# Kernel tuning notes

Hardware: AMD Instinct MI355X
Metric: run time of the kernel (lower is better)

The kernel has to match this reference:

```python
import jax, jax.numpy as jnp
import numpy as np
import math

B, S, HID = 2, 2048, 512
NH, NKV, HD = 8, 2, 256
ROT = 64          # partial_rotary_factor 0.25 * head_dim 256
ROPE_THETA = 10000000.0
EPS = 1e-6


def _rms_norm(x, w):
    # zero-centered RMSNorm: x / rms * (1 + w)
    rms = jnp.sqrt(jnp.mean(x * x, axis=-1, keepdims=True) + EPS)
    return x / rms * (1.0 + w)


def _partial_rope(x, cos, sin):
    # x: [B,S,H,HD]; cos/sin: [S, ROT//2]
    xr = x[..., :ROT].reshape(*x.shape[:-1], ROT // 2, 2)
    a, b = xr[..., 0], xr[..., 1]
    c = cos[None, :, None, :]
    s = sin[None, :, None, :]
    rot = jnp.stack([a * c - b * s, a * s + b * c], axis=-1).reshape(*x.shape[:-1], ROT)
    return jnp.concatenate([rot, x[..., ROT:]], axis=-1)


def setup_inputs() -> dict:
    key = jax.random.key(0)
    ks = jax.random.split(key, 6)
    x = jax.random.normal(ks[0], (B, S, HID), dtype=jnp.float32)
    # real RoPE frequencies
    inv_freq = 1.0 / (ROPE_THETA ** (np.arange(0, ROT, 2, dtype=np.float32) / ROT))
    t = np.arange(S, dtype=np.float32)
    angles = np.outer(t, inv_freq)  # [S, ROT//2]
    cos = jnp.asarray(np.cos(angles), dtype=jnp.float32)
    sin = jnp.asarray(np.sin(angles), dtype=jnp.float32)
    # additive causal mask [S,S]
    mask = jnp.where(jnp.tril(jnp.ones((S, S), dtype=bool)), 0.0, -1e9).astype(jnp.float32)
    sc = 0.02
    wq = jax.random.normal(ks[1], (HID, NH * HD), dtype=jnp.float32) * sc
    wk = jax.random.normal(ks[2], (HID, NKV * HD), dtype=jnp.float32) * sc
    wv = jax.random.normal(ks[3], (HID, NKV * HD), dtype=jnp.float32) * sc
    wo = jax.random.normal(ks[4], (NH * HD, HID), dtype=jnp.float32) * sc
    q_norm_w = jnp.zeros((HD,), dtype=jnp.float32)
    k_norm_w = jnp.zeros((HD,), dtype=jnp.float32)
    return {"x": x, "cos": cos, "sin": sin, "mask": mask,
            "wq": wq, "wk": wk, "wv": wv, "wo": wo,
            "q_norm_w": q_norm_w, "k_norm_w": k_norm_w}


def reference(x, cos, sin, mask, wq, wk, wv, wo, q_norm_w, k_norm_w):
    b, s, _ = x.shape
    groups = NH // NKV
    q = (x @ wq).reshape(b, s, NH, HD)
    k = (x @ wk).reshape(b, s, NKV, HD)
    v = (x @ wv).reshape(b, s, NKV, HD)
    q = _partial_rope(_rms_norm(q, q_norm_w), cos, sin)
    k = _partial_rope(_rms_norm(k, k_norm_w), cos, sin)
    # GQA: broadcast kv heads to NH
    k = jnp.repeat(k, groups, axis=2)  # [b,s,NH,HD]
    v = jnp.repeat(v, groups, axis=2)
    scale = math.sqrt(HD)
    scores = jnp.einsum('bqhd,bkhd->bhqk', q, k) / scale
    scores = scores + mask[None, None, :, :]
    attn = jax.nn.softmax(scores, axis=-1)
    out = jnp.einsum('bhqk,bkhd->bqhd', attn, v).reshape(b, s, NH * HD)
    return out @ wo
```

## Files before the change

### kernel.cpp

```cpp
#include <hip/hip_runtime.h>

#define S_LEN 2048
#define NHQ 8
#define NKV 2
#define HD 256
#define KVB 32

typedef __attribute__((ext_vector_type(8))) short bf16x8;
typedef __attribute__((ext_vector_type(4))) short bf16x4;
typedef __attribute__((ext_vector_type(4))) float f32x4;
typedef __attribute__((ext_vector_type(16))) float f32x16;
typedef __attribute__((ext_vector_type(4))) unsigned u32x4;

__device__ __forceinline__ short f2bf(float f) {
    unsigned u = __builtin_bit_cast(unsigned, f);
    u += 0x7FFFu + ((u >> 16) & 1u);
    return (short)(u >> 16);
}
__device__ __forceinline__ float bf2f(short s) {
    unsigned u = ((unsigned)(unsigned short)s) << 16;
    return __builtin_bit_cast(float, u);
}
__device__ __forceinline__ unsigned cvtpk(float a, float b) {
    unsigned r;
    asm("v_cvt_pk_bf16_f32 %0, %1, %2" : "=v"(r) : "v"(a), "v"(b));
    return r;
}
__device__ __forceinline__ void gload16(const short* g, short* l) {
    __builtin_amdgcn_global_load_lds((const __attribute__((address_space(1))) unsigned*)g,
                                     (__attribute__((address_space(3))) unsigned*)l, 16, 0, 0);
}
__device__ __forceinline__ float bperm(int srclane, float v) {
    return __builtin_bit_cast(float,
        __builtin_amdgcn_ds_bpermute(srclane * 4, __builtin_bit_cast(int, v)));
}

__global__ __launch_bounds__(256) void cvt_kernel(const float* __restrict__ in,
                                                  short* __restrict__ out, int n) {
    int i = (blockIdx.x * 256 + threadIdx.x) * 4;
    if (i + 3 < n) {
        float4 f = *(const float4*)(in + i);
        bf16x4 o;
        o[0] = f2bf(f.x); o[1] = f2bf(f.y); o[2] = f2bf(f.z); o[3] = f2bf(f.w);
        *(bf16x4*)(out + i) = o;
    }
}

__global__ __launch_bounds__(256) void wt_kernel(const float* __restrict__ in,
                                                 short* __restrict__ out,
                                                 int K, int N) {
    __shared__ short tile[64][72];
    int n0 = blockIdx.x * 64, k0 = blockIdx.y * 64;
    int t = threadIdx.x;
    #pragma unroll
    for (int i = 0; i < 16; i++) {
        int flat = i * 256 + t; int r = flat >> 6, c = flat & 63;
        tile[r][c] = f2bf(in[(long)(k0 + r) * N + n0 + c]);
    }
    __syncthreads();
    #pragma unroll
    for (int i = 0; i < 16; i++) {
        int flat = i * 256 + t; int r = flat >> 6, c = flat & 63;
        out[(long)(n0 + r) * K + k0 + c] = tile[c][r];
    }
}

template<int BN, int WRITE_BF16>
__global__ __launch_bounds__(256) void gemm_bt(const short* __restrict__ A,
                                               const short* __restrict__ Bt,
                                               void* __restrict__ Cv,
                                               int M, int N, int K) {
    constexpr int NI = BN / 32;
    __shared__ short As[128 * 32];
    __shared__ short Bs[BN * 32];
    const int t = threadIdx.x;
    const int lane = t & 63, w = t >> 6;
    const int lr = lane & 15, lg = lane >> 4;
    const int m0 = blockIdx.y * 128, n0 = blockIdx.x * BN;
    const int wm = (w >> 1) * 64, wn = (w & 1) * (BN / 2);

    f32x4 acc[4][NI];
    #pragma unroll
    for (int i = 0; i < 4; i++)
        #pragma unroll
        for (int j = 0; j < NI; j++) acc[i][j] = (f32x4){0.f, 0.f, 0.f, 0.f};

    for (int k0 = 0; k0 < K; k0 += 32) {
        __syncthreads();
        #pragma unroll
        for (int r = 0; r < 2; r++) {
            int sbase = r * 2048 + w * 512;
            int srow = (sbase + lane * 8) >> 5, scol = (sbase + lane * 8) & 31;
            gload16(A + (long)(m0 + srow) * K + k0 + scol, &As[sbase]);
        }
        #pragma unroll
        for (int r = 0; r < BN / 64; r++) {
            int sbase = r * 2048 + w * 512;
            int srow = (sbase + lane * 8) >> 5, scol = (sbase + lane * 8) & 31;
            gload16(Bt + (long)(n0 + srow) * K + k0 + scol, &Bs[sbase]);
        }
        __syncthreads();
        bf16x8 af[4], bfr[NI];
        #pragma unroll
        for (int mi = 0; mi < 4; mi++)
            af[mi] = *(const bf16x8*)&As[(wm + mi * 16 + lr) * 32 + lg * 8];
        #pragma unroll
        for (int ni = 0; ni < NI; ni++)
            bfr[ni] = *(const bf16x8*)&Bs[(wn + ni * 16 + lr) * 32 + lg * 8];
        #pragma unroll
        for (int mi = 0; mi < 4; mi++)
            #pragma unroll
            for (int ni = 0; ni < NI; ni++)
                acc[mi][ni] = __builtin_amdgcn_mfma_f32_16x16x32_bf16(af[mi], bfr[ni], acc[mi][ni], 0, 0, 0);
    }
    #pragma unroll
    for (int mi = 0; mi < 4; mi++)
    #pragma unroll
    for (int ni = 0; ni < NI; ni++)
    #pragma unroll
    for (int r = 0; r < 4; r++) {
        long row = m0 + wm + mi * 16 + lg * 4 + r;
        long col = n0 + wn + ni * 16 + lr;
        float v = acc[mi][ni][r];
        if (WRITE_BF16) ((short*)Cv)[row * N + col] = f2bf(v);
        else            ((float*)Cv)[row * N + col] = v;
    }
}

__global__ __launch_bounds__(256) void norm_rope_kernel(
    const short* __restrict__ in, short* __restrict__ out,
    const float* __restrict__ w, const float* __restrict__ cosb,
    const float* __restrict__ sinb, int H, long ldin, long cofs,
    long ob, long oh, long os, float scale) {
    int vec = blockIdx.x * 4 + (threadIdx.x >> 6);
    int lane = threadIdx.x & 63;
    int token = vec / H, head = vec % H;
    int b = token / S_LEN, s = token % S_LEN;

    bf16x4 xv = *(const bf16x4*)(in + (long)token * ldin + cofs + head * 256 + lane * 4);
    float x0 = bf2f(xv[0]), x1 = bf2f(xv[1]), x2 = bf2f(xv[2]), x3 = bf2f(xv[3]);
    float ss = x0 * x0 + x1 * x1 + x2 * x2 + x3 * x3;
    #pragma unroll
    for (int m = 1; m < 64; m <<= 1) ss += __shfl_xor(ss, m);
    float inv = rsqrtf(ss * (1.f / 256.f) + 1e-6f);

    float4 wv = *(const float4*)(w + lane * 4);
    float y0 = x0 * inv * (1.f + wv.x);
    float y1 = x1 * inv * (1.f + wv.y);
    float y2 = x2 * inv * (1.f + wv.z);
    float y3 = x3 * inv * (1.f + wv.w);

    if (lane < 16) {
        float2 c = *(const float2*)&cosb[s * 32 + lane * 2];
        float2 sn = *(const float2*)&sinb[s * 32 + lane * 2];
        float a0 = y0 * c.x - y1 * sn.x, b0 = y0 * sn.x + y1 * c.x;
        float a1 = y2 * c.y - y3 * sn.y, b1 = y2 * sn.y + y3 * c.y;
        y0 = a0; y1 = b0; y2 = a1; y3 = b1;
    }
    y0 *= scale; y1 *= scale; y2 *= scale; y3 *= scale;
    long oidx = (long)b * ob + (long)head * oh + (long)s * os + lane * 4;
    bf16x4 o; o[0] = f2bf(y0); o[1] = f2bf(y1); o[2] = f2bf(y2); o[3] = f2bf(y3);
    *(bf16x4*)(out + oidx) = o;
}

__global__ __launch_bounds__(256) void transpose_v_kernel(const short* __restrict__ C,
                                                          short* __restrict__ vr) {
    __shared__ short tile[64][65];
    int s0 = blockIdx.x * 64, d0 = blockIdx.y * 64;
    int bkv = blockIdx.z; int b = bkv >> 1, kv = bkv & 1;
    int t = threadIdx.x;
    #pragma unroll
    for (int i = 0; i < 16; i++) {
        int flat = i * 256 + t; int si = flat >> 6, di = flat & 63;
        tile[si][di] = C[(long)(b * S_LEN + s0 + si) * 3072 + 2560 + kv * 256 + d0 + di];
    }
    __syncthreads();
    #pragma unroll
    for (int i = 0; i < 16; i++) {
        int flat = i * 256 + t; int di = flat >> 6, si = flat & 63;
        vr[(long)(bkv * 256 + d0 + di) * S_LEN + s0 + si] = tile[si][di];
    }
}

__global__ __launch_bounds__(256, 2) void flash_kernel(const short* __restrict__ Cq,
                                                       const short* __restrict__ Kt,
                                                       const short* __restrict__ Vt,
                                                       short* __restrict__ O,
                                                       const float* __restrict__ qnw,
                                                       const float* __restrict__ cosb,
                                                       const float* __restrict__ sinb) {
    __shared__ __align__(16) char smem[66048];

    int idx = blockIdx.x;
    int half = idx >> 8, rm = idx & 255;
    int xcd = rm & 7, slot = rm >> 3;
    int bh = xcd * 2 + (slot & 1);
    int jj = slot >> 1;
    int j  = half ? jj : (31 - jj);
    int h = bh & 7, b = bh >> 3;
    int kv = h >> 2;
    int t = threadIdx.x, lane = t & 63, w = t >> 6;
    int g = w >> 1, p = w & 1;
    int ln = lane & 31, hi = lane >> 5;
    int q0 = j * 64 + g * 32;
    int qg = q0 + ln;

    const short* Kb = Kt + (long)(b * NKV + kv) * S_LEN * HD;
    const short* Vb = Vt + (long)(b * NKV + kv) * HD * S_LEN;

    auto stageK = [&](int ph2) {
        #pragma unroll
        for (int pp = 0; pp < 2; pp++) {
            int k0s = (2 * ph2 + pp) * KVB;
            short* Ktile = (short*)(smem + pp * 16384);
            #pragma unroll
            for (int c = 0; c < 4; c++) {
                int o = c * 4096 + w * 1024 + lane * 16;
                int key = o >> 9, db = o & 511;
                gload16(Kb + (long)(k0s + key) * HD + ((db ^ ((key & 7) << 4)) >> 1),
                        Ktile + (c * 4096 + w * 1024) / 2);
            }
        }
    };
    auto stageV = [&](int ph2) {
        #pragma unroll
        for (int pp = 0; pp < 2; pp++) {
            int k0s = (2 * ph2 + pp) * KVB;
            short* Vtile = (short*)(smem + 32768 + pp * 16384);
            #pragma unroll
            for (int c = 0; c < 4; c++) {
                int o = c * 4096 + w * 1024 + lane * 16;
                int d = o >> 6, kb = o & 63;
                gload16(Vb + (long)d * S_LEN + k0s + ((kb ^ ((d & 6) << 3)) >> 1),
                        Vtile + (c * 4096 + w * 1024) / 2);
            }
        }
    };

    stageK(0); stageV(0);

    bf16x8 qf[16];
    {
        const short* qrow = Cq + (long)(b * S_LEN + qg) * 3072 + h * 256 + hi * 8;
        #pragma unroll
        for (int dc = 0; dc < 16; dc++) qf[dc] = *(const bf16x8*)&qrow[dc * 16];
        float ss = 0.f;
        #pragma unroll
        for (int dc = 0; dc < 16; dc++)
            #pragma unroll
            for (int e = 0; e < 8; e++) { float v = bf2f(qf[dc][e]); ss += v * v; }
        ss += __shfl_xor(ss, 32);
        float inv = rsqrtf(ss * (1.f / 256.f) + 1e-6f);
        #pragma unroll
        for (int dc = 0; dc < 16; dc++) {
            float y[8];
            float4 w0 = *(const float4*)&qnw[dc * 16 + hi * 8];
            float4 w1 = *(const float4*)&qnw[dc * 16 + hi * 8 + 4];
            y[0] = bf2f(qf[dc][0]) * inv * (1.f + w0.x);
            y[1] = bf2f(qf[dc][1]) * inv * (1.f + w0.y);
            y[2] = bf2f(qf[dc][2]) * inv * (1.f + w0.z);
            y[3] = bf2f(qf[dc][3]) * inv * (1.f + w0.w);
            y[4] = bf2f(qf[dc][4]) * inv * (1.f + w1.x);
            y[5] = bf2f(qf[dc][5]) * inv * (1.f + w1.y);
            y[6] = bf2f(qf[dc][6]) * inv * (1.f + w1.z);
            y[7] = bf2f(qf[dc][7]) * inv * (1.f + w1.w);
            if (dc < 4) {
                float4 c4 = *(const float4*)&cosb[qg * 32 + dc * 8 + hi * 4];
                float4 s4 = *(const float4*)&sinb[qg * 32 + dc * 8 + hi * 4];
                float a, bb;
                a = y[0]; bb = y[1]; y[0] = a * c4.x - bb * s4.x; y[1] = a * s4.x + bb * c4.x;
                a = y[2]; bb = y[3]; y[2] = a * c4.y - bb * s4.y; y[3] = a * s4.y + bb * c4.y;
                a = y[4]; bb = y[5]; y[4] = a * c4.z - bb * s4.z; y[5] = a * s4.z + bb * c4.z;
                a = y[6]; bb = y[7]; y[6] = a * c4.w - bb * s4.w; y[7] = a * s4.w + bb * c4.w;
            }
            bf16x8 o;
            #pragma unroll
            for (int e = 0; e < 8; e++) o[e] = f2bf(y[e] * 0.0625f);
            qf[dc] = o;
        }
    }

    f32x16 acc[8];
    #pragma unroll
    for (int i = 0; i < 8; i++)
        #pragma unroll
        for (int r = 0; r < 16; r++) acc[i][r] = 0.f;
    float m = -1e30f, l = 0.f;

    for (int ph = 0; ph <= j; ph++) {
        const bool last = (ph == j);
        asm volatile("s_waitcnt vmcnt(8)" ::: "memory");
        __builtin_amdgcn_s_barrier();
        int k0 = (2 * ph + p) * KVB;
        bool act = (k0 <= q0 + 31);

        f32x16 s;
        if (act) {
            const char* Ks = (const char*)smem + p * 16384;
            f32x16 sA, sB;
            #pragma unroll
            for (int r = 0; r < 16; r++) { sA[r] = 0.f; sB[r] = 0.f; }
            __builtin_amdgcn_s_setprio(1);
            #pragma unroll
            for (int dc = 0; dc < 16; dc += 2) {
                int kb0 = (dc * 32 + hi * 16) ^ ((ln & 7) << 4);
                int kb1 = ((dc + 1) * 32 + hi * 16) ^ ((ln & 7) << 4);
                bf16x8 kf0 = *(const bf16x8*)(Ks + ln * 512 + kb0);
                bf16x8 kf1 = *(const bf16x8*)(Ks + ln * 512 + kb1);
                sA = __builtin_amdgcn_mfma_f32_32x32x16_bf16(kf0, qf[dc],     sA, 0, 0, 0);
                sB = __builtin_amdgcn_mfma_f32_32x32x16_bf16(kf1, qf[dc + 1], sB, 0, 0, 0);
            }
            __builtin_amdgcn_s_setprio(0);
            #pragma unroll
            for (int r = 0; r < 16; r++) s[r] = sA[r] + sB[r];
        }
        __builtin_amdgcn_s_barrier();
        if (!last) stageK(ph + 1);
        __builtin_amdgcn_sched_barrier(0);

        bf16x8 pa0, pa1;
        if (act) {
            if (k0 + KVB - 1 > q0) {
                #pragma unroll
                for (int r = 0; r < 16; r++) {
                    int key_g = k0 + (r & 3) + 8 * (r >> 2) + 4 * hi;
                    if (key_g > qg) s[r] = -1e30f;
                }
            }
            float mt = s[0];
            #pragma unroll
            for (int r = 1; r < 16; r++) mt = fmaxf(mt, s[r]);
            mt = fmaxf(mt, __shfl_xor(mt, 32));
            float mn = m;
            if (!__all(mt <= m + 8.f)) {
                mn = fmaxf(m, mt);
                float f = __expf(m - mn);
                m = mn;
                float fr[16];
                #pragma unroll
                for (int r = 0; r < 16; r++)
                    fr[r] = bperm((r & 3) + 8 * (r >> 2) + 4 * hi, f);
                #pragma unroll
                for (int i = 0; i < 8; i++)
                    #pragma unroll
                    for (int r = 0; r < 16; r++) acc[i][r] *= fr[r];
                l *= f;
            }
            float pr[16], ps = 0.f;
            #pragma unroll
            for (int r = 0; r < 16; r++) { pr[r] = __expf(s[r] - mn); ps += pr[r]; }
            ps += __shfl_xor(ps, 32);
            l += ps;

            unsigned pw[8];
            #pragma unroll
            for (int kc = 0; kc < 2; kc++) {
                unsigned X = cvtpk(pr[kc * 8 + 0], pr[kc * 8 + 1]);
                unsigned Y = cvtpk(pr[kc * 8 + 4], pr[kc * 8 + 5]);
                unsigned Z = cvtpk(pr[kc * 8 + 2], pr[kc * 8 + 3]);
                unsigned W = cvtpk(pr[kc * 8 + 6], pr[kc * 8 + 7]);
                asm volatile("v_permlane32_swap_b32 %0, %1" : "+v"(X), "+v"(Y));
                asm volatile("v_permlane32_swap_b32 %0, %1" : "+v"(Z), "+v"(W));
                pw[kc * 4 + 0] = X; pw[kc * 4 + 1] = Z;
                pw[kc * 4 + 2] = Y; pw[kc * 4 + 3] = W;
            }
            u32x4 w0v = {pw[0], pw[1], pw[2], pw[3]};
            u32x4 w1v = {pw[4], pw[5], pw[6], pw[7]};
            pa0 = __builtin_bit_cast(bf16x8, w0v);
            pa1 = __builtin_bit_cast(bf16x8, w1v);
        }

        if (last) { asm volatile("s_waitcnt vmcnt(0)" ::: "memory"); }
        else      { asm volatile("s_waitcnt vmcnt(8)" ::: "memory"); }
        __builtin_amdgcn_s_barrier();

        if (act) {
            const char* Vs = (const char*)smem + 32768 + p * 16384;
            __builtin_amdgcn_s_setprio(1);
            #pragma unroll
            for (int db = 0; db < 8; db++) {
                int drow = db * 32 + ln;
                int sw = (drow & 6) << 3;
                bf16x8 vf0 = *(const bf16x8*)(Vs + drow * 64 + ((hi * 16) ^ sw));
                bf16x8 vf1 = *(const bf16x8*)(Vs + drow * 64 + ((32 + hi * 16) ^ sw));
                acc[db] = __builtin_amdgcn_mfma_f32_32x32x16_bf16(pa0, vf0, acc[db], 0, 0, 0);
                acc[db] = __builtin_amdgcn_mfma_f32_32x32x16_bf16(pa1, vf1, acc[db], 0, 0, 0);
            }
            __builtin_amdgcn_s_setprio(0);
        }
        __builtin_amdgcn_s_barrier();
        if (!last) stageV(ph + 1);
    }

    float* accb = (float*)smem;
    float* mlb  = (float*)(smem + 65536);
    if (p == 1) {
        #pragma unroll
        for (int db = 0; db < 8; db++)
            #pragma unroll
            for (int r = 0; r < 16; r++)
                accb[g * 8192 + (db * 16 + r) * 64 + hi * 32 + ln] = acc[db][r];
        if (hi == 0) { mlb[g * 32 + ln] = m; mlb[64 + g * 32 + ln] = l; }
    }
    __syncthreads();
    if (p == 0) {
        float m1 = mlb[g * 32 + ln], l1 = mlb[64 + g * 32 + ln];
        float M  = fmaxf(m, m1);
        float f0 = __expf(m - M), f1 = __expf(m1 - M);
        float lt = l * f0 + l1 * f1;
        float w0 = f0 / lt, w1 = f1 / lt;
        float fr0[16], fr1[16];
        #pragma unroll
        for (int r = 0; r < 16; r++) {
            int crow = (r & 3) + 8 * (r >> 2) + 4 * hi;
            fr0[r] = bperm(crow, w0);
            fr1[r] = bperm(crow, w1);
        }
        #pragma unroll
        for (int db = 0; db < 8; db++)
            #pragma unroll
            for (int r = 0; r < 16; r++) {
                float a1 = accb[g * 8192 + (db * 16 + r) * 64 + hi * 32 + ln];
                int qrow = q0 + (r & 3) + 8 * (r >> 2) + 4 * hi;
                O[(long)(b * S_LEN + qrow) * 2048 + h * HD + db * 32 + ln] =
                    f2bf(acc[db][r] * fr0[r] + a1 * fr1[r]);
            }
    }
}

extern "C" void kernel_launch(void* const* d_in, const int* in_sizes, int n_in,
                              void* d_out, int out_size, void* d_ws, size_t ws_size,
                              hipStream_t stream) {
    const float* x    = (const float*)d_in[0];
    const float* cosb = (const float*)d_in[1];
    const float* sinb = (const float*)d_in[2];
    const float* wq   = (const float*)d_in[4];
    const float* wk   = (const float*)d_in[5];
    const float* wv   = (const float*)d_in[6];
    const float* wo   = (const float*)d_in[7];
    const float* qnw  = (const float*)d_in[8];
    const float* knw  = (const float*)d_in[9];
    float* out = (float*)d_out;

    char* ws = (char*)d_ws;
    short* xb   = (short*)(ws + 0);
    short* wfus = (short*)(ws + 4194304);
    short* wot  = (short*)(ws + 7340032);
    short* C    = (short*)(ws + 9437184);
    short* ao   = (short*)(ws + 34603008);
    short* kr   = (short*)(ws + 51380224);
    short* vr   = (short*)(ws + 55574528);

    cvt_kernel<<<2048, 256, 0, stream>>>(x, xb, 2097152);
    wt_kernel<<<dim3(32, 8), 256, 0, stream>>>(wq, wfus,              512, 2048);
    wt_kernel<<<dim3(8, 8),  256, 0, stream>>>(wk, wfus + 2048 * 512, 512, 512);
    wt_kernel<<<dim3(8, 8),  256, 0, stream>>>(wv, wfus + 2560 * 512, 512, 512);
    wt_kernel<<<dim3(8, 32), 256, 0, stream>>>(wo, wot, 2048, 512);

    gemm_bt<128, 1><<<dim3(24, 32), 256, 0, stream>>>(xb, wfus, C, 4096, 3072, 512);

    norm_rope_kernel<<<2048, 256, 0, stream>>>(C, kr, knw, cosb, sinb, 2,
                                               3072L, 2048L, 1048576L, 524288L, 256L, 1.0f);
    transpose_v_kernel<<<dim3(32, 4, 4), 256, 0, stream>>>(C, vr);

    flash_kernel<<<512, 256, 0, stream>>>(C, kr, vr, ao, qnw, cosb, sinb);

    gemm_bt<64, 0><<<dim3(8, 32), 256, 0, stream>>>(ao, wot, out, 4096, 512, 2048);
}
```

Baseline: 201.8 us.

## Merge K and V staging into one load phase per iteration

Replaces the split K/V staging, where K for the next step was loaded during softmax and V during the PV phase, with one combined stage issued after each step's full compute. Each iteration now waits for all loads, computes QK, softmax and PV without an intermediate barrier, then issues the next K and V loads together. This drops two barriers and a waitcnt per iteration, but removes the overlap between next-tile loads and the current compute, since the wait is vmcnt(0) right after the loads are issued.

```diff
diff --git a/kernel.cpp b/kernel.cpp
--- a/kernel.cpp
+++ b/kernel.cpp
@@ -208,28 +208,18 @@
     const short* Kb = Kt + (long)(b * NKV + kv) * S_LEN * HD;
     const short* Vb = Vt + (long)(b * NKV + kv) * HD * S_LEN;
 
-    auto stageK = [&](int ph2) {
+    auto stage = [&](int ph2) {
         #pragma unroll
         for (int pp = 0; pp < 2; pp++) {
             int k0s = (2 * ph2 + pp) * KVB;
             short* Ktile = (short*)(smem + pp * 16384);
+            short* Vtile = (short*)(smem + 32768 + pp * 16384);
             #pragma unroll
             for (int c = 0; c < 4; c++) {
                 int o = c * 4096 + w * 1024 + lane * 16;
                 int key = o >> 9, db = o & 511;
                 gload16(Kb + (long)(k0s + key) * HD + ((db ^ ((key & 7) << 4)) >> 1),
                         Ktile + (c * 4096 + w * 1024) / 2);
-            }
-        }
-    };
-    auto stageV = [&](int ph2) {
-        #pragma unroll
-        for (int pp = 0; pp < 2; pp++) {
-            int k0s = (2 * ph2 + pp) * KVB;
-            short* Vtile = (short*)(smem + 32768 + pp * 16384);
-            #pragma unroll
-            for (int c = 0; c < 4; c++) {
-                int o = c * 4096 + w * 1024 + lane * 16;
                 int d = o >> 6, kb = o & 63;
                 gload16(Vb + (long)d * S_LEN + k0s + ((kb ^ ((d & 6) << 3)) >> 1),
                         Vtile + (c * 4096 + w * 1024) / 2);
@@ -237,7 +227,7 @@
         }
     };
 
-    stageK(0); stageV(0);
+    stage(0);
 
     bf16x8 qf[16];
     {
@@ -284,112 +274,100 @@
     #pragma unroll
     for (int i = 0; i < 8; i++)
         #pragma unroll
-        for (int r = 0; r < 16; r++) acc[i][r] = 0.f;
+        for (int jj2 = 0; jj2 < 16; jj2++) acc[i][jj2] = 0.f;
     float m = -1e30f, l = 0.f;
 
+    auto compute = [&](int k0) {
+        const char* Ks = (const char*)smem + p * 16384;
+        const char* Vs = (const char*)smem + 32768 + p * 16384;
+        f32x16 sA, sB;
+        #pragma unroll
+        for (int r = 0; r < 16; r++) { sA[r] = 0.f; sB[r] = 0.f; }
+        __builtin_amdgcn_s_setprio(1);
+        #pragma unroll
+        for (int dc = 0; dc < 16; dc += 2) {
+            int kb0 = (dc * 32 + hi * 16) ^ ((ln & 7) << 4);
+            int kb1 = ((dc + 1) * 32 + hi * 16) ^ ((ln & 7) << 4);
+            bf16x8 kf0 = *(const bf16x8*)(Ks + ln * 512 + kb0);
+            bf16x8 kf1 = *(const bf16x8*)(Ks + ln * 512 + kb1);
+            sA = __builtin_amdgcn_mfma_f32_32x32x16_bf16(kf0, qf[dc],     sA, 0, 0, 0);
+            sB = __builtin_amdgcn_mfma_f32_32x32x16_bf16(kf1, qf[dc + 1], sB, 0, 0, 0);
+        }
+        __builtin_amdgcn_s_setprio(0);
+        f32x16 s;
+        #pragma unroll
+        for (int r = 0; r < 16; r++) s[r] = sA[r] + sB[r];
+
+        if (k0 + KVB - 1 > q0) {
+            #pragma unroll
+            for (int r = 0; r < 16; r++) {
+                int key_g = k0 + (r & 3) + 8 * (r >> 2) + 4 * hi;
+                if (key_g > qg) s[r] = -1e30f;
+            }
+        }
+        float mt = s[0];
+        #pragma unroll
+        for (int r = 1; r < 16; r++) mt = fmaxf(mt, s[r]);
+        mt = fmaxf(mt, __shfl_xor(mt, 32));
+        float mn = m;
+        if (!__all(mt <= m + 8.f)) {
+            mn = fmaxf(m, mt);
+            float f = __expf(m - mn);
+            m = mn;
+            float fr[16];
+            #pragma unroll
+            for (int r = 0; r < 16; r++)
+                fr[r] = bperm((r & 3) + 8 * (r >> 2) + 4 * hi, f);
+            #pragma unroll
+            for (int i = 0; i < 8; i++)
+                #pragma unroll
+                for (int r = 0; r < 16; r++) acc[i][r] *= fr[r];
+            l *= f;
+        }
+        float pr[16], ps = 0.f;
+        #pragma unroll
+        for (int r = 0; r < 16; r++) { pr[r] = __expf(s[r] - mn); ps += pr[r]; }
+        ps += __shfl_xor(ps, 32);
+        l += ps;
+
+        unsigned pw[8];
+        #pragma unroll
+        for (int kc = 0; kc < 2; kc++) {
+            unsigned X = cvtpk(pr[kc * 8 + 0], pr[kc * 8 + 1]);
+            unsigned Y = cvtpk(pr[kc * 8 + 4], pr[kc * 8 + 5]);
+            unsigned Z = cvtpk(pr[kc * 8 + 2], pr[kc * 8 + 3]);
+            unsigned W = cvtpk(pr[kc * 8 + 6], pr[kc * 8 + 7]);
+            asm volatile("v_permlane32_swap_b32 %0, %1" : "+v"(X), "+v"(Y));
+            asm volatile("v_permlane32_swap_b32 %0, %1" : "+v"(Z), "+v"(W));
+            pw[kc * 4 + 0] = X; pw[kc * 4 + 1] = Z;
+            pw[kc * 4 + 2] = Y; pw[kc * 4 + 3] = W;
+        }
+        u32x4 w0v = {pw[0], pw[1], pw[2], pw[3]};
+        u32x4 w1v = {pw[4], pw[5], pw[6], pw[7]};
+        bf16x8 pa0 = __builtin_bit_cast(bf16x8, w0v);
+        bf16x8 pa1 = __builtin_bit_cast(bf16x8, w1v);
+
+        __builtin_amdgcn_s_setprio(1);
+        #pragma unroll
+        for (int db = 0; db < 8; db++) {
+            int drow = db * 32 + ln;
+            int sw = (drow & 6) << 3;
+            bf16x8 vf0 = *(const bf16x8*)(Vs + drow * 64 + ((hi * 16) ^ sw));
+            bf16x8 vf1 = *(const bf16x8*)(Vs + drow * 64 + ((32 + hi * 16) ^ sw));
+            acc[db] = __builtin_amdgcn_mfma_f32_32x32x16_bf16(pa0, vf0, acc[db], 0, 0, 0);
+            acc[db] = __builtin_amdgcn_mfma_f32_32x32x16_bf16(pa1, vf1, acc[db], 0, 0, 0);
+        }
+        __builtin_amdgcn_s_setprio(0);
+    };
+
     for (int ph = 0; ph <= j; ph++) {
-        const bool last = (ph == j);
-        asm volatile("s_waitcnt vmcnt(8)" ::: "memory");
+        asm volatile("s_waitcnt vmcnt(0)" ::: "memory");
         __builtin_amdgcn_s_barrier();
         int k0 = (2 * ph + p) * KVB;
-        bool act = (k0 <= q0 + 31);
-
-        f32x16 s;
-        if (act) {
-            const char* Ks = (const char*)smem + p * 16384;
-            f32x16 sA, sB;
-            #pragma unroll
-            for (int r = 0; r < 16; r++) { sA[r] = 0.f; sB[r] = 0.f; }
-            __builtin_amdgcn_s_setprio(1);
-            #pragma unroll
-            for (int dc = 0; dc < 16; dc += 2) {
-                int kb0 = (dc * 32 + hi * 16) ^ ((ln & 7) << 4);
-                int kb1 = ((dc + 1) * 32 + hi * 16) ^ ((ln & 7) << 4);
-                bf16x8 kf0 = *(const bf16x8*)(Ks + ln * 512 + kb0);
-                bf16x8 kf1 = *(const bf16x8*)(Ks + ln * 512 + kb1);
-                sA = __builtin_amdgcn_mfma_f32_32x32x16_bf16(kf0, qf[dc],     sA, 0, 0, 0);
-                sB = __builtin_amdgcn_mfma_f32_32x32x16_bf16(kf1, qf[dc + 1], sB, 0, 0, 0);
-            }
-            __builtin_amdgcn_s_setprio(0);
-            #pragma unroll
-            for (int r = 0; r < 16; r++) s[r] = sA[r] + sB[r];
-        }
+        if (k0 <= q0 + 31) compute(k0);
         __builtin_amdgcn_s_barrier();
-        if (!last) stageK(ph + 1);
+        if (ph < j) stage(ph + 1);
         __builtin_amdgcn_sched_barrier(0);
-
-        bf16x8 pa0, pa1;
-        if (act) {
-            if (k0 + KVB - 1 > q0) {
-                #pragma unroll
-                for (int r = 0; r < 16; r++) {
-                    int key_g = k0 + (r & 3) + 8 * (r >> 2) + 4 * hi;
-                    if (key_g > qg) s[r] = -1e30f;
-                }
-            }
-            float mt = s[0];
-            #pragma unroll
-            for (int r = 1; r < 16; r++) mt = fmaxf(mt, s[r]);
-            mt = fmaxf(mt, __shfl_xor(mt, 32));
-            float mn = m;
-            if (!__all(mt <= m + 8.f)) {
-                mn = fmaxf(m, mt);
-                float f = __expf(m - mn);
-                m = mn;
-                float fr[16];
-                #pragma unroll
-                for (int r = 0; r < 16; r++)
-                    fr[r] = bperm((r & 3) + 8 * (r >> 2) + 4 * hi, f);
-                #pragma unroll
-                for (int i = 0; i < 8; i++)
-                    #pragma unroll
-                    for (int r = 0; r < 16; r++) acc[i][r] *= fr[r];
-                l *= f;
-            }
-            float pr[16], ps = 0.f;
-            #pragma unroll
-            for (int r = 0; r < 16; r++) { pr[r] = __expf(s[r] - mn); ps += pr[r]; }
-            ps += __shfl_xor(ps, 32);
-            l += ps;
-
-            unsigned pw[8];
-            #pragma unroll
-            for (int kc = 0; kc < 2; kc++) {
-                unsigned X = cvtpk(pr[kc * 8 + 0], pr[kc * 8 + 1]);
-                unsigned Y = cvtpk(pr[kc * 8 + 4], pr[kc * 8 + 5]);
-                unsigned Z = cvtpk(pr[kc * 8 + 2], pr[kc * 8 + 3]);
-                unsigned W = cvtpk(pr[kc * 8 + 6], pr[kc * 8 + 7]);
-                asm volatile("v_permlane32_swap_b32 %0, %1" : "+v"(X), "+v"(Y));
-                asm volatile("v_permlane32_swap_b32 %0, %1" : "+v"(Z), "+v"(W));
-                pw[kc * 4 + 0] = X; pw[kc * 4 + 1] = Z;
-                pw[kc * 4 + 2] = Y; pw[kc * 4 + 3] = W;
-            }
-            u32x4 w0v = {pw[0], pw[1], pw[2], pw[3]};
-            u32x4 w1v = {pw[4], pw[5], pw[6], pw[7]};
-            pa0 = __builtin_bit_cast(bf16x8, w0v);
-            pa1 = __builtin_bit_cast(bf16x8, w1v);
-        }
-
-        if (last) { asm volatile("s_waitcnt vmcnt(0)" ::: "memory"); }
-        else      { asm volatile("s_waitcnt vmcnt(8)" ::: "memory"); }
-        __builtin_amdgcn_s_barrier();
-
-        if (act) {
-            const char* Vs = (const char*)smem + 32768 + p * 16384;
-            __builtin_amdgcn_s_setprio(1);
-            #pragma unroll
-            for (int db = 0; db < 8; db++) {
-                int drow = db * 32 + ln;
-                int sw = (drow & 6) << 3;
-                bf16x8 vf0 = *(const bf16x8*)(Vs + drow * 64 + ((hi * 16) ^ sw));
-                bf16x8 vf1 = *(const bf16x8*)(Vs + drow * 64 + ((32 + hi * 16) ^ sw));
-                acc[db] = __builtin_amdgcn_mfma_f32_32x32x16_bf16(pa0, vf0, acc[db], 0, 0, 0);
-                acc[db] = __builtin_amdgcn_mfma_f32_32x32x16_bf16(pa1, vf1, acc[db], 0, 0, 0);
-            }
-            __builtin_amdgcn_s_setprio(0);
-        }
-        __builtin_amdgcn_s_barrier();
-        if (!last) stageV(ph + 1);
     }
 
     float* accb = (float*)smem;
```

After: 276.8 us. 37.2% more time.
